# Kernel tuning notes

Hardware: AMD Instinct MI355X
Metric: run time of the kernel (lower is better)

Reference implementation:

```python
import jax, jax.numpy as jnp
import numpy as np

NUM_HEADS = 12
STEP_SIZE = 3

def softmax_1(a):
    # exp(a_i) / (1 + sum_j exp(a_j)), numerically stable
    m = jnp.maximum(jnp.max(a, axis=-1, keepdims=True), 0.0)
    e = jnp.exp(a - m)
    return e / (jnp.exp(-m) + jnp.sum(e, axis=-1, keepdims=True))

def setup_inputs() -> dict:
    key = jax.random.key(0)
    ks = jax.random.split(key, 7)
    B, N, C, L = 16, 4096, 768, 16
    s = C ** -0.5
    return {
        "x": jax.random.normal(ks[0], (B, N, C), dtype=jnp.float32),
        "query": jax.random.normal(ks[1], (1, L, C), dtype=jnp.float32),
        "Wq": jax.random.normal(ks[2], (C, C), dtype=jnp.float32) * s,
        "Wk": jax.random.normal(ks[3], (C, C), dtype=jnp.float32) * s,
        "Wv": jax.random.normal(ks[4], (C, C), dtype=jnp.float32) * s,
        "Wproj": jax.random.normal(ks[5], (C, C), dtype=jnp.float32) * s,
        "b_proj": jnp.zeros((C,), dtype=jnp.float32),
    }

def reference(x, query, Wq, Wk, Wv, Wproj, b_proj):
    B, N, C = x.shape
    H = NUM_HEADS
    hd = C // H
    L = query.shape[1]
    scale = hd ** -0.5
    # learned queries broadcast over batch
    queries = jnp.broadcast_to(query, (B, L, C))
    q = (queries @ Wq.T).reshape(B, L, H, hd).transpose(0, 2, 1, 3)  # [B,H,L,hd]
    k = (x @ Wk.T).reshape(B, N, H, hd).transpose(0, 2, 1, 3)        # [B,H,N,hd]
    v = k  # Hopfield update: state retrieves against stored patterns k
    for _ in range(STEP_SIZE):
        qs = q * scale
        attn = jnp.einsum('bhld,bhnd->bhln', qs, k)  # [B,H,L,N]
        attn = softmax_1(attn)
        q = jnp.einsum('bhln,bhnd->bhld', attn, v)   # [B,H,L,hd]
    out = q.transpose(0, 2, 1, 3).reshape(B, L, C)
    out = out @ Wv.T          # self.v output projection (no bias)
    out = out @ Wproj.T + b_proj  # self.proj
    return out
```

## Files before the change

### kernel.cpp

```cpp
#include <hip/hip_runtime.h>


typedef float  float4v  __attribute__((ext_vector_type(4)));
typedef short  short4v  __attribute__((ext_vector_type(4)));
typedef short  short8v  __attribute__((ext_vector_type(8)));
typedef unsigned int uint4v __attribute__((ext_vector_type(4)));
typedef short8v bf16x8;

#define NC 4

__device__ __forceinline__ unsigned short f2bf_hi(float f){
  unsigned int u = __float_as_uint(f);
  u += 0x7fffu + ((u >> 16) & 1u);
  return (unsigned short)(u >> 16);
}
__device__ __forceinline__ float bf2f(unsigned short h){
  return __uint_as_float(((unsigned int)h) << 16);
}
__device__ __forceinline__ unsigned int packbf(float v){
  unsigned short hh = f2bf_hi(v);
  return (unsigned)hh | ((unsigned)f2bf_hi(v - bf2f(hh)) << 16);
}

__global__ __launch_bounds__(256)
void cvt_planar_kernel(const float* __restrict__ src, unsigned short* __restrict__ dh,
                       unsigned short* __restrict__ dl){
  size_t idx = (size_t)blockIdx.x*256 + threadIdx.x;
  float4v v = ((const float4v*)src)[idx];
  short4v h4, l4;
  #pragma unroll
  for(int e=0;e<4;e++){
    unsigned short hh = f2bf_hi(v[e]);
    h4[e] = (short)hh;
    l4[e] = (short)f2bf_hi(v[e] - bf2f(hh));
  }
  ((short4v*)dh)[idx] = h4;
  ((short4v*)dl)[idx] = l4;
}

__global__ __launch_bounds__(256)
void q0_kernel(const float* __restrict__ query, const float* __restrict__ wq,
               float* __restrict__ q0){
  int idx = blockIdx.x*256 + threadIdx.x;
  int l = idx / 768, c = idx - l*768;
  const float* qr = query + l*768;
  const float* wr = wq + (size_t)c*768;
  float s = 0.f;
  for(int j=0;j<768;j+=4){
    float4v a  = *(const float4v*)(qr+j);
    float4v w4 = *(const float4v*)(wr+j);
    s += a[0]*w4[0]+a[1]*w4[1]+a[2]*w4[2]+a[3]*w4[3];
  }
  q0[idx] = s;
}

__global__ __launch_bounds__(256, 4)
void gemm_k_kernel(const float* __restrict__ x, const unsigned short* __restrict__ wh,
                   const unsigned short* __restrict__ wl, unsigned int* __restrict__ kout){
  __shared__ unsigned short Ah[128*40], Al[128*40];
  const int tid  = threadIdx.x;
  const int id   = blockIdx.x;
  const int xcd  = id & 7, slot = id >> 3;
  const int bml  = slot / 6;
  const int bn   = slot - bml*6;
  const int bm   = xcd*64 + bml;
  const int wave = tid >> 6, lane = tid & 63, quad = lane >> 4, l16 = lane & 15;

  float4v acc[8][2];
  #pragma unroll
  for(int i=0;i<8;i++)
    #pragma unroll
    for(int j=0;j<2;j++) acc[i][j] = (float4v){0.f,0.f,0.f,0.f};

  const float* xA = x + (size_t)bm*128*768;
  const unsigned short* wbh = wh + (size_t)(bn*128 + wave*32 + l16)*768 + quad*8;
  const unsigned short* wbl = wl + (size_t)(bn*128 + wave*32 + l16)*768 + quad*8;

  for(int k0=0;k0<768;k0+=32){
    bf16x8 b_h[2], b_l[2];
    #pragma unroll
    for(int j=0;j<2;j++){
      b_h[j] = *(const bf16x8*)(wbh + (size_t)j*16*768 + k0);
      b_l[j] = *(const bf16x8*)(wbl + (size_t)j*16*768 + k0);
    }
    __syncthreads();
    #pragma unroll
    for(int i=0;i<2;i++){
      int fi = tid + i*256;
      int row = fi >> 2, c8 = fi & 3;
      const float* sp = xA + (size_t)row*768 + k0 + c8*8;
      float4v va = *(const float4v*)sp;
      float4v vb = *(const float4v*)(sp + 4);
      short8v hv, lv;
      #pragma unroll
      for(int e=0;e<4;e++){
        unsigned short hh = f2bf_hi(va[e]);
        hv[e] = (short)hh; lv[e] = (short)f2bf_hi(va[e] - bf2f(hh));
        unsigned short hh2 = f2bf_hi(vb[e]);
        hv[e+4] = (short)hh2; lv[e+4] = (short)f2bf_hi(vb[e] - bf2f(hh2));
      }
      *(short8v*)(Ah + row*40 + c8*8) = hv;
      *(short8v*)(Al + row*40 + c8*8) = lv;
    }
    __syncthreads();

    #pragma unroll
    for(int i=0;i<8;i++){
      const int ar = i*16 + l16;
      bf16x8 a_h = *(const bf16x8*)(Ah + ar*40 + quad*8);
      bf16x8 a_l = *(const bf16x8*)(Al + ar*40 + quad*8);
      #pragma unroll
      for(int j=0;j<2;j++){
        acc[i][j] = __builtin_amdgcn_mfma_f32_16x16x32_bf16(a_h, b_h[j], acc[i][j],0,0,0);
        acc[i][j] = __builtin_amdgcn_mfma_f32_16x16x32_bf16(a_l, b_h[j], acc[i][j],0,0,0);
        acc[i][j] = __builtin_amdgcn_mfma_f32_16x16x32_bf16(a_h, b_l[j], acc[i][j],0,0,0);
      }
    }
  }
  const size_t cbase = (size_t)(bm*128)*768 + bn*128 + wave*32;
  #pragma unroll
  for(int i=0;i<8;i++)
    #pragma unroll
    for(int j=0;j<2;j++)
      #pragma unroll
      for(int r=0;r<4;r++)
        kout[cbase + (size_t)(i*16 + quad*4 + r)*768 + j*16 + l16] = packbf(acc[i][j][r]);
}

__global__ __launch_bounds__(256, 3)
void attn_step_kernel(const unsigned int* __restrict__ kbuf, const float* __restrict__ qsrc,
                      long qb_stride, float* __restrict__ qacc, float* __restrict__ lacc){
  __shared__ unsigned int knd[128*68];
  __shared__ float red[4][16];

  const int tid  = threadIdx.x;
  const int c    = blockIdx.x;
  const int h    = blockIdx.y;
  const int b    = blockIdx.z;
  const int wave = tid >> 6, lane = tid & 63, quad = lane >> 4, l16 = lane & 15;

  const unsigned int* kb = kbuf + ((size_t)b*4096 + (size_t)c*(4096/NC))*768 + h*64;

  const float* qp = qsrc + (size_t)b*qb_stride + (size_t)l16*768 + h*64;
  bf16x8 qh[2], ql[2];
  #pragma unroll
  for(int s = 0; s < 2; ++s){
    float4v v0 = *(const float4v*)(qp + s*32 + quad*8);
    float4v v1 = *(const float4v*)(qp + s*32 + quad*8 + 4);
    #pragma unroll
    for(int e = 0; e < 8; ++e){
      float v = (e < 4 ? v0[e] : v1[e-4]) * 0.125f;
      unsigned short hh = f2bf_hi(v);
      qh[s][e] = (short)hh;
      ql[s][e] = (short)f2bf_hi(v - bf2f(hh));
    }
  }

  float4v acc[4];
  #pragma unroll
  for(int j=0;j<4;j++) acc[j] = (float4v){0.f,0.f,0.f,0.f};
  float lsum = 0.f;

  const int prow = tid >> 1, pcol = (tid & 1)*32;
  const int T = (4096/NC)/128;
  uint4v pf[8];
  {
    const unsigned int* src = kb + (size_t)prow*768 + pcol;
    #pragma unroll
    for(int g=0; g<8; ++g) pf[g] = *(const uint4v*)(src + g*4);
  }

  const int rA = wave*32 + 8*(l16 >> 2) + (l16 & 3);

  for(int t = 0; t < T; ++t){
    #pragma unroll
    for(int g=0; g<8; ++g) *(uint4v*)(knd + prow*68 + pcol + g*4) = pf[g];
    __syncthreads();
    if(t+1 < T){
      const unsigned int* src = kb + (size_t)((t+1)*128 + prow)*768 + pcol;
      #pragma unroll
      for(int g=0; g<8; ++g) pf[g] = *(const uint4v*)(src + g*4);
    }

    float4v s1 = (float4v){0.f,0.f,0.f,0.f};
    float4v s2 = (float4v){0.f,0.f,0.f,0.f};
    #pragma unroll
    for(int s = 0; s < 2; ++s){
      const unsigned int* a1p = knd + rA*68 + s*32 + quad*8;
      const unsigned int* a2p = a1p + 4*68;
      uint4v w0 = *(const uint4v*)a1p;
      uint4v w1 = *(const uint4v*)(a1p + 4);
      uint4v u0 = *(const uint4v*)a2p;
      uint4v u1 = *(const uint4v*)(a2p + 4);
      bf16x8 a1h, a1l, a2h, a2l;
      #pragma unroll
      for(int j = 0; j < 4; ++j){
        a1h[j]   = (short)(w0[j] & 0xffffu);  a1l[j]   = (short)(w0[j] >> 16);
        a1h[j+4] = (short)(w1[j] & 0xffffu);  a1l[j+4] = (short)(w1[j] >> 16);
        a2h[j]   = (short)(u0[j] & 0xffffu);  a2l[j]   = (short)(u0[j] >> 16);
        a2h[j+4] = (short)(u1[j] & 0xffffu);  a2l[j+4] = (short)(u1[j] >> 16);
      }
      s1 = __builtin_amdgcn_mfma_f32_16x16x32_bf16(a1h, qh[s], s1, 0,0,0);
      s1 = __builtin_amdgcn_mfma_f32_16x16x32_bf16(a1l, qh[s], s1, 0,0,0);
      s1 = __builtin_amdgcn_mfma_f32_16x16x32_bf16(a1h, ql[s], s1, 0,0,0);
      s2 = __builtin_amdgcn_mfma_f32_16x16x32_bf16(a2h, qh[s], s2, 0,0,0);
      s2 = __builtin_amdgcn_mfma_f32_16x16x32_bf16(a2l, qh[s], s2, 0,0,0);
      s2 = __builtin_amdgcn_mfma_f32_16x16x32_bf16(a2h, ql[s], s2, 0,0,0);
    }

    bf16x8 pa_h, pa_l;
    #pragma unroll
    for(int e = 0; e < 4; ++e){
      float v = __expf(s1[e]);
      lsum += v;
      unsigned short hh = f2bf_hi(v);
      pa_h[e] = (short)hh;
      pa_l[e] = (short)f2bf_hi(v - bf2f(hh));
      float v2 = __expf(s2[e]);
      lsum += v2;
      unsigned short hh2 = f2bf_hi(v2);
      pa_h[e+4] = (short)hh2;
      pa_l[e+4] = (short)f2bf_hi(v2 - bf2f(hh2));
    }

    const unsigned int* bbase = knd + (size_t)(wave*32 + quad*8)*68 + l16;
    #pragma unroll
    for(int j = 0; j < 4; ++j){
      const unsigned int* bp = bbase + j*16;
      bf16x8 kbh, kbl;
      #pragma unroll
      for(int e = 0; e < 8; ++e){
        unsigned int w = bp[e*68];
        kbh[e] = (short)(w & 0xffffu);
        kbl[e] = (short)(w >> 16);
      }
      acc[j] = __builtin_amdgcn_mfma_f32_16x16x32_bf16(pa_h, kbh, acc[j], 0,0,0);
      acc[j] = __builtin_amdgcn_mfma_f32_16x16x32_bf16(pa_l, kbh, acc[j], 0,0,0);
      acc[j] = __builtin_amdgcn_mfma_f32_16x16x32_bf16(pa_h, kbl, acc[j], 0,0,0);
    }
    __syncthreads();
  }

  lsum += __shfl_xor(lsum, 16);
  lsum += __shfl_xor(lsum, 32);
  if(quad == 0) red[wave][l16] = lsum;
  __syncthreads();
  if(tid < 16){
    float tot = red[0][tid] + red[1][tid] + red[2][tid] + red[3][tid];
    atomicAdd(&lacc[(b*12 + h)*16 + tid], tot);
  }
  #pragma unroll
  for(int j = 0; j < 4; ++j)
    #pragma unroll
    for(int r = 0; r < 4; ++r)
      atomicAdd(&qacc[(size_t)(b*16 + quad*4 + r)*768 + h*64 + j*16 + l16], acc[j][r]);
}

__global__ __launch_bounds__(256)
void attn_norm_kernel(float* __restrict__ qacc, float* __restrict__ lacc,
                      float* __restrict__ qcur){
  __shared__ float lt[16];
  const int bh = blockIdx.x, b = bh/12, h = bh - (bh/12)*12, tid = threadIdx.x;
  if(tid < 16) lt[tid] = 1.f + lacc[bh*16 + tid];
  __syncthreads();
  if(tid < 16) lacc[bh*16 + tid] = 0.f;
  for(int idx = tid; idx < 1024; idx += 256){
    int l = idx >> 6, d = idx & 63;
    size_t a = (size_t)(b*16 + l)*768 + h*64 + d;
    qcur[a] = qacc[a] / lt[l];
    qacc[a] = 0.f;
  }
}

__global__ __launch_bounds__(256)
void proj_kernel(const float* __restrict__ inp, const float* __restrict__ w,
                 const float* __restrict__ bias, float* __restrict__ out){
  __shared__ float rows[4*768];
  const int r0 = blockIdx.x*4;
  const int c  = blockIdx.y*256 + threadIdx.x;
  for(int j = threadIdx.x; j < 4*768; j += 256) rows[j] = inp[(size_t)r0*768 + j];
  __syncthreads();
  const float* wr = w + (size_t)c*768;
  float a0=0.f, a1=0.f, a2=0.f, a3=0.f;
  for(int j=0;j<768;j+=4){
    float4v w4 = *(const float4v*)(wr+j);
    float4v r0v = *(const float4v*)(rows+j);
    float4v r1v = *(const float4v*)(rows+768+j);
    float4v r2v = *(const float4v*)(rows+1536+j);
    float4v r3v = *(const float4v*)(rows+2304+j);
    #pragma unroll
    for(int e=0;e<4;e++){
      a0 += r0v[e]*w4[e]; a1 += r1v[e]*w4[e];
      a2 += r2v[e]*w4[e]; a3 += r3v[e]*w4[e];
    }
  }
  const float bb = bias ? bias[c] : 0.f;
  out[(size_t)(r0+0)*768 + c] = a0 + bb;
  out[(size_t)(r0+1)*768 + c] = a1 + bb;
  out[(size_t)(r0+2)*768 + c] = a2 + bb;
  out[(size_t)(r0+3)*768 + c] = a3 + bb;
}

extern "C" void kernel_launch(void* const* d_in, const int* in_sizes, int n_in,
                              void* d_out, int out_size, void* d_ws, size_t ws_size,
                              hipStream_t stream){
  const float* x     = (const float*)d_in[0];
  const float* query = (const float*)d_in[1];
  const float* Wq    = (const float*)d_in[2];
  const float* Wk    = (const float*)d_in[3];
  const float* Wv    = (const float*)d_in[4];
  const float* Wproj = (const float*)d_in[5];
  const float* bproj = (const float*)d_in[6];
  float* out = (float*)d_out;

  char* ws = (char*)d_ws;
  unsigned int*   kbuf = (unsigned int*)(ws);
  float*          qcur = (float*)(ws + 201326592);
  float*          q0   = (float*)(ws + 202113024);
  char*           R    = ws + 202162176;
  unsigned short* wkh  = (unsigned short*)(R);
  unsigned short* wkl  = (unsigned short*)(R + 1179648);
  float*          qacc = (float*)(R);
  float*          lacc = (float*)(R + 786432);
  float*          out1 = (float*)(R);

  cvt_planar_kernel<<<576, 256, 0, stream>>>(Wk, wkh, wkl);
  q0_kernel<<<48, 256, 0, stream>>>(query, Wq, q0);
  gemm_k_kernel<<<3072, 256, 0, stream>>>(x, wkh, wkl, kbuf);

  hipMemsetAsync(qacc, 0, 786432 + 12288, stream);
  dim3 sg(NC, 12, 16);
  attn_step_kernel<<<sg, 256, 0, stream>>>(kbuf, q0,   0,       qacc, lacc);
  attn_norm_kernel<<<192, 256, 0, stream>>>(qacc, lacc, qcur);
  attn_step_kernel<<<sg, 256, 0, stream>>>(kbuf, qcur, 16*768,  qacc, lacc);
  attn_norm_kernel<<<192, 256, 0, stream>>>(qacc, lacc, qcur);
  attn_step_kernel<<<sg, 256, 0, stream>>>(kbuf, qcur, 16*768,  qacc, lacc);
  attn_norm_kernel<<<192, 256, 0, stream>>>(qacc, lacc, qcur);

  proj_kernel<<<dim3(64, 3), 256, 0, stream>>>(qcur, Wv, nullptr, out1);
  proj_kernel<<<dim3(64, 3), 256, 0, stream>>>(out1, Wproj, bproj, out);
}
```

Baseline: 749.2 us.

## Store K head-major and pre-split x to bf16 planes for LDS-free GEMM

The K projection output is now written in a per-(batch, head) contiguous layout, so each attention step reads fully contiguous 128x64 tiles instead of strided rows. The K GEMM drops the shared-memory staging of x and loads A and B fragments directly from global memory, using a 2x2 wave tiling with a larger per-wave register tile. When the workspace is large enough, x is first converted once into hi/lo bf16 planes so the GEMM does no per-tile conversion; otherwise a variant converts x inline. The trade is an extra full pass over x, about 200MB of extra workspace traffic, and higher register pressure.

```diff
diff --git a/kernel.cpp b/kernel.cpp
--- a/kernel.cpp
+++ b/kernel.cpp
@@ -54,10 +54,10 @@
   q0[idx] = s;
 }
 
-__global__ __launch_bounds__(256, 4)
-void gemm_k_kernel(const float* __restrict__ x, const unsigned short* __restrict__ wh,
-                   const unsigned short* __restrict__ wl, unsigned int* __restrict__ kout){
-  __shared__ unsigned short Ah[128*40], Al[128*40];
+__global__ __launch_bounds__(256, 3)
+void gemm_k_pre_kernel(const unsigned short* __restrict__ xh, const unsigned short* __restrict__ xl,
+                       const unsigned short* __restrict__ wh, const unsigned short* __restrict__ wl,
+                       unsigned int* __restrict__ khead){
   const int tid  = threadIdx.x;
   const int id   = blockIdx.x;
   const int xcd  = id & 7, slot = id >> 3;
@@ -65,70 +65,121 @@
   const int bn   = slot - bml*6;
   const int bm   = xcd*64 + bml;
   const int wave = tid >> 6, lane = tid & 63, quad = lane >> 4, l16 = lane & 15;
-
-  float4v acc[8][2];
-  #pragma unroll
-  for(int i=0;i<8;i++)
-    #pragma unroll
-    for(int j=0;j<2;j++) acc[i][j] = (float4v){0.f,0.f,0.f,0.f};
-
-  const float* xA = x + (size_t)bm*128*768;
-  const unsigned short* wbh = wh + (size_t)(bn*128 + wave*32 + l16)*768 + quad*8;
-  const unsigned short* wbl = wl + (size_t)(bn*128 + wave*32 + l16)*768 + quad*8;
+  const int wr   = wave >> 1, wc = wave & 1;
+
+  float4v acc[4][4];
+  #pragma unroll
+  for(int i=0;i<4;i++)
+    #pragma unroll
+    for(int j=0;j<4;j++) acc[i][j] = (float4v){0.f,0.f,0.f,0.f};
+
+  const size_t aoff = (size_t)(bm*128 + wr*64 + l16)*768 + quad*8;
+  const size_t boff = (size_t)(bn*128 + wc*64 + l16)*768 + quad*8;
+  const unsigned short* pah = xh + aoff;
+  const unsigned short* pal = xl + aoff;
+  const unsigned short* pbh = wh + boff;
+  const unsigned short* pbl = wl + boff;
 
   for(int k0=0;k0<768;k0+=32){
-    bf16x8 b_h[2], b_l[2];
-    #pragma unroll
-    for(int j=0;j<2;j++){
-      b_h[j] = *(const bf16x8*)(wbh + (size_t)j*16*768 + k0);
-      b_l[j] = *(const bf16x8*)(wbl + (size_t)j*16*768 + k0);
-    }
-    __syncthreads();
-    #pragma unroll
-    for(int i=0;i<2;i++){
-      int fi = tid + i*256;
-      int row = fi >> 2, c8 = fi & 3;
-      const float* sp = xA + (size_t)row*768 + k0 + c8*8;
+    bf16x8 ah[4], al[4], bh[4], bl[4];
+    #pragma unroll
+    for(int i=0;i<4;i++){
+      ah[i] = *(const bf16x8*)(pah + (size_t)i*16*768 + k0);
+      al[i] = *(const bf16x8*)(pal + (size_t)i*16*768 + k0);
+      bh[i] = *(const bf16x8*)(pbh + (size_t)i*16*768 + k0);
+      bl[i] = *(const bf16x8*)(pbl + (size_t)i*16*768 + k0);
+    }
+    #pragma unroll
+    for(int i=0;i<4;i++)
+      #pragma unroll
+      for(int j=0;j<4;j++){
+        acc[i][j] = __builtin_amdgcn_mfma_f32_16x16x32_bf16(ah[i], bh[j], acc[i][j],0,0,0);
+        acc[i][j] = __builtin_amdgcn_mfma_f32_16x16x32_bf16(al[i], bh[j], acc[i][j],0,0,0);
+        acc[i][j] = __builtin_amdgcn_mfma_f32_16x16x32_bf16(ah[i], bl[j], acc[i][j],0,0,0);
+      }
+  }
+  const int b     = bm >> 5;
+  const int h     = bn*2 + wc;
+  const int nbase = (bm & 31)*128 + wr*64;
+  unsigned int* kout = khead + (size_t)(b*12 + h)*4096*64;
+  #pragma unroll
+  for(int i=0;i<4;i++)
+    #pragma unroll
+    for(int j=0;j<4;j++)
+      #pragma unroll
+      for(int r=0;r<4;r++){
+        const int n = nbase + i*16 + quad*4 + r;
+        kout[(size_t)n*64 + j*16 + l16] = packbf(acc[i][j][r]);
+      }
+}
+
+__global__ __launch_bounds__(256, 3)
+void gemm_k_fly_kernel(const float* __restrict__ x,
+                       const unsigned short* __restrict__ wh, const unsigned short* __restrict__ wl,
+                       unsigned int* __restrict__ khead){
+  const int tid  = threadIdx.x;
+  const int id   = blockIdx.x;
+  const int xcd  = id & 7, slot = id >> 3;
+  const int bml  = slot / 6;
+  const int bn   = slot - bml*6;
+  const int bm   = xcd*64 + bml;
+  const int wave = tid >> 6, lane = tid & 63, quad = lane >> 4, l16 = lane & 15;
+  const int wr   = wave >> 1, wc = wave & 1;
+
+  float4v acc[4][4];
+  #pragma unroll
+  for(int i=0;i<4;i++)
+    #pragma unroll
+    for(int j=0;j<4;j++) acc[i][j] = (float4v){0.f,0.f,0.f,0.f};
+
+  const float* pax = x + (size_t)(bm*128 + wr*64 + l16)*768 + quad*8;
+  const size_t boff = (size_t)(bn*128 + wc*64 + l16)*768 + quad*8;
+  const unsigned short* pbh = wh + boff;
+  const unsigned short* pbl = wl + boff;
+
+  for(int k0=0;k0<768;k0+=32){
+    bf16x8 ah[4], al[4], bh[4], bl[4];
+    #pragma unroll
+    for(int i=0;i<4;i++){
+      const float* sp = pax + (size_t)i*16*768 + k0;
       float4v va = *(const float4v*)sp;
       float4v vb = *(const float4v*)(sp + 4);
-      short8v hv, lv;
       #pragma unroll
       for(int e=0;e<4;e++){
         unsigned short hh = f2bf_hi(va[e]);
-        hv[e] = (short)hh; lv[e] = (short)f2bf_hi(va[e] - bf2f(hh));
+        ah[i][e] = (short)hh; al[i][e] = (short)f2bf_hi(va[e] - bf2f(hh));
         unsigned short hh2 = f2bf_hi(vb[e]);
-        hv[e+4] = (short)hh2; lv[e+4] = (short)f2bf_hi(vb[e] - bf2f(hh2));
-      }
-      *(short8v*)(Ah + row*40 + c8*8) = hv;
-      *(short8v*)(Al + row*40 + c8*8) = lv;
-    }
-    __syncthreads();
-
-    #pragma unroll
-    for(int i=0;i<8;i++){
-      const int ar = i*16 + l16;
-      bf16x8 a_h = *(const bf16x8*)(Ah + ar*40 + quad*8);
-      bf16x8 a_l = *(const bf16x8*)(Al + ar*40 + quad*8);
-      #pragma unroll
-      for(int j=0;j<2;j++){
-        acc[i][j] = __builtin_amdgcn_mfma_f32_16x16x32_bf16(a_h, b_h[j], acc[i][j],0,0,0);
-        acc[i][j] = __builtin_amdgcn_mfma_f32_16x16x32_bf16(a_l, b_h[j], acc[i][j],0,0,0);
-        acc[i][j] = __builtin_amdgcn_mfma_f32_16x16x32_bf16(a_h, b_l[j], acc[i][j],0,0,0);
-      }
-    }
-  }
-  const size_t cbase = (size_t)(bm*128)*768 + bn*128 + wave*32;
-  #pragma unroll
-  for(int i=0;i<8;i++)
-    #pragma unroll
-    for(int j=0;j<2;j++)
-      #pragma unroll
-      for(int r=0;r<4;r++)
-        kout[cbase + (size_t)(i*16 + quad*4 + r)*768 + j*16 + l16] = packbf(acc[i][j][r]);
+        ah[i][e+4] = (short)hh2; al[i][e+4] = (short)f2bf_hi(vb[e] - bf2f(hh2));
+      }
+      bh[i] = *(const bf16x8*)(pbh + (size_t)i*16*768 + k0);
+      bl[i] = *(const bf16x8*)(pbl + (size_t)i*16*768 + k0);
+    }
+    #pragma unroll
+    for(int i=0;i<4;i++)
+      #pragma unroll
+      for(int j=0;j<4;j++){
+        acc[i][j] = __builtin_amdgcn_mfma_f32_16x16x32_bf16(ah[i], bh[j], acc[i][j],0,0,0);
+        acc[i][j] = __builtin_amdgcn_mfma_f32_16x16x32_bf16(al[i], bh[j], acc[i][j],0,0,0);
+        acc[i][j] = __builtin_amdgcn_mfma_f32_16x16x32_bf16(ah[i], bl[j], acc[i][j],0,0,0);
+      }
+  }
+  const int b     = bm >> 5;
+  const int h     = bn*2 + wc;
+  const int nbase = (bm & 31)*128 + wr*64;
+  unsigned int* kout = khead + (size_t)(b*12 + h)*4096*64;
+  #pragma unroll
+  for(int i=0;i<4;i++)
+    #pragma unroll
+    for(int j=0;j<4;j++)
+      #pragma unroll
+      for(int r=0;r<4;r++){
+        const int n = nbase + i*16 + quad*4 + r;
+        kout[(size_t)n*64 + j*16 + l16] = packbf(acc[i][j][r]);
+      }
 }
 
 __global__ __launch_bounds__(256, 3)
-void attn_step_kernel(const unsigned int* __restrict__ kbuf, const float* __restrict__ qsrc,
+void attn_step_kernel(const unsigned int* __restrict__ khead, const float* __restrict__ qsrc,
                       long qb_stride, float* __restrict__ qacc, float* __restrict__ lacc){
   __shared__ unsigned int knd[128*68];
   __shared__ float red[4][16];
@@ -139,7 +190,7 @@
   const int b    = blockIdx.z;
   const int wave = tid >> 6, lane = tid & 63, quad = lane >> 4, l16 = lane & 15;
 
-  const unsigned int* kb = kbuf + ((size_t)b*4096 + (size_t)c*(4096/NC))*768 + h*64;
+  const unsigned int* kb = khead + ((size_t)(b*12 + h)*4096 + (size_t)c*1024)*64;
 
   const float* qp = qsrc + (size_t)b*qb_stride + (size_t)l16*768 + h*64;
   bf16x8 qh[2], ql[2];
@@ -161,25 +212,26 @@
   for(int j=0;j<4;j++) acc[j] = (float4v){0.f,0.f,0.f,0.f};
   float lsum = 0.f;
 
-  const int prow = tid >> 1, pcol = (tid & 1)*32;
-  const int T = (4096/NC)/128;
+  const int srow = tid >> 4, scol = (tid & 15)*4;
+  const int T = (1024)/128;
   uint4v pf[8];
   {
-    const unsigned int* src = kb + (size_t)prow*768 + pcol;
-    #pragma unroll
-    for(int g=0; g<8; ++g) pf[g] = *(const uint4v*)(src + g*4);
+    const unsigned int* src = kb + tid*4;
+    #pragma unroll
+    for(int g=0; g<8; ++g) pf[g] = *(const uint4v*)(src + g*1024);
   }
 
   const int rA = wave*32 + 8*(l16 >> 2) + (l16 & 3);
 
   for(int t = 0; t < T; ++t){
     #pragma unroll
-    for(int g=0; g<8; ++g) *(uint4v*)(knd + prow*68 + pcol + g*4) = pf[g];
+    for(int g=0; g<8; ++g)
+      *(uint4v*)(knd + (g*16 + srow)*68 + scol) = pf[g];
     __syncthreads();
     if(t+1 < T){
-      const unsigned int* src = kb + (size_t)((t+1)*128 + prow)*768 + pcol;
-      #pragma unroll
-      for(int g=0; g<8; ++g) pf[g] = *(const uint4v*)(src + g*4);
+      const unsigned int* src = kb + (size_t)(t+1)*8192 + tid*4;
+      #pragma unroll
+      for(int g=0; g<8; ++g) pf[g] = *(const uint4v*)(src + g*1024);
     }
 
     float4v s1 = (float4v){0.f,0.f,0.f,0.f};
@@ -313,30 +365,65 @@
   const float* bproj = (const float*)d_in[6];
   float* out = (float*)d_out;
 
+  const size_t XB   = 100663296;
+  const size_t KB_  = 201326592;
+  const size_t PRE_NEED = 2*XB + KB_ + 786432 + 49152 + 2359296;
+
   char* ws = (char*)d_ws;
-  unsigned int*   kbuf = (unsigned int*)(ws);
-  float*          qcur = (float*)(ws + 201326592);
-  float*          q0   = (float*)(ws + 202113024);
-  char*           R    = ws + 202162176;
-  unsigned short* wkh  = (unsigned short*)(R);
-  unsigned short* wkl  = (unsigned short*)(R + 1179648);
-  float*          qacc = (float*)(R);
-  float*          lacc = (float*)(R + 786432);
-  float*          out1 = (float*)(R);
-
-  cvt_planar_kernel<<<576, 256, 0, stream>>>(Wk, wkh, wkl);
-  q0_kernel<<<48, 256, 0, stream>>>(query, Wq, q0);
-  gemm_k_kernel<<<3072, 256, 0, stream>>>(x, wkh, wkl, kbuf);
-
-  hipMemsetAsync(qacc, 0, 786432 + 12288, stream);
   dim3 sg(NC, 12, 16);
-  attn_step_kernel<<<sg, 256, 0, stream>>>(kbuf, q0,   0,       qacc, lacc);
-  attn_norm_kernel<<<192, 256, 0, stream>>>(qacc, lacc, qcur);
-  attn_step_kernel<<<sg, 256, 0, stream>>>(kbuf, qcur, 16*768,  qacc, lacc);
-  attn_norm_kernel<<<192, 256, 0, stream>>>(qacc, lacc, qcur);
-  attn_step_kernel<<<sg, 256, 0, stream>>>(kbuf, qcur, 16*768,  qacc, lacc);
-  attn_norm_kernel<<<192, 256, 0, stream>>>(qacc, lacc, qcur);
-
-  proj_kernel<<<dim3(64, 3), 256, 0, stream>>>(qcur, Wv, nullptr, out1);
-  proj_kernel<<<dim3(64, 3), 256, 0, stream>>>(out1, Wproj, bproj, out);
-}
+
+  if(ws_size >= PRE_NEED){
+    unsigned short* xh    = (unsigned short*)(ws);
+    unsigned short* xl    = (unsigned short*)(ws + XB);
+    unsigned int*   khead = (unsigned int*)  (ws + 2*XB);
+    float*          qcur  = (float*)(ws + 2*XB + KB_);
+    float*          q0    = (float*)(ws + 2*XB + KB_ + 786432);
+    char*           R     = ws + 2*XB + KB_ + 786432 + 49152;
+    unsigned short* wkh   = (unsigned short*)(R);
+    unsigned short* wkl   = (unsigned short*)(R + 1179648);
+    float*          qacc  = (float*)(R);
+    float*          lacc  = (float*)(R + 786432);
+    float*          out1  = (float*)(R);
+
+    cvt_planar_kernel<<<576, 256, 0, stream>>>(Wk, wkh, wkl);
+    cvt_planar_kernel<<<49152, 256, 0, stream>>>(x, xh, xl);
+    q0_kernel<<<48, 256, 0, stream>>>(query, Wq, q0);
+    gemm_k_pre_kernel<<<3072, 256, 0, stream>>>(xh, xl, wkh, wkl, khead);
+
+    hipMemsetAsync(qacc, 0, 786432 + 12288, stream);
+    attn_step_kernel<<<sg, 256, 0, stream>>>(khead, q0,   0,       qacc, lacc);
+    attn_norm_kernel<<<192, 256, 0, stream>>>(qacc, lacc, qcur);
+    attn_step_kernel<<<sg, 256, 0, stream>>>(khead, qcur, 16*768,  qacc, lacc);
+    attn_norm_kernel<<<192, 256, 0, stream>>>(qacc, lacc, qcur);
+    attn_step_kernel<<<sg, 256, 0, stream>>>(khead, qcur, 16*768,  qacc, lacc);
+    attn_norm_kernel<<<192, 256, 0, stream>>>(qacc, lacc, qcur);
+
+    proj_kernel<<<dim3(64, 3), 256, 0, stream>>>(qcur, Wv, nullptr, out1);
+    proj_kernel<<<dim3(64, 3), 256, 0, stream>>>(out1, Wproj, bproj, out);
+  } else {
+    unsigned int*   khead = (unsigned int*)(ws);
+    float*          qcur  = (float*)(ws + 201326592);
+    float*          q0    = (float*)(ws + 202113024);
+    char*           R     = ws + 202162176;
+    unsigned short* wkh   = (unsigned short*)(R);
+    unsigned short* wkl   = (unsigned short*)(R + 1179648);
+    float*          qacc  = (float*)(R);
+    float*          lacc  = (float*)(R + 786432);
+    float*          out1  = (float*)(R);
+
+    cvt_planar_kernel<<<576, 256, 0, stream>>>(Wk, wkh, wkl);
+    q0_kernel<<<48, 256, 0, stream>>>(query, Wq, q0);
+    gemm_k_fly_kernel<<<3072, 256, 0, stream>>>(x, wkh, wkl, khead);
+
+    hipMemsetAsync(qacc, 0, 786432 + 12288, stream);
+    attn_step_kernel<<<sg, 256, 0, stream>>>(khead, q0,   0,       qacc, lacc);
+    attn_norm_kernel<<<192, 256, 0, stream>>>(qacc, lacc, qcur);
+    attn_step_kernel<<<sg, 256, 0, stream>>>(khead, qcur, 16*768,  qacc, lacc);
+    attn_norm_kernel<<<192, 256, 0, stream>>>(qacc, lacc, qcur);
+    attn_step_kernel<<<sg, 256, 0, stream>>>(khead, qcur, 16*768,  qacc, lacc);
+    attn_norm_kernel<<<192, 256, 0, stream>>>(qacc, lacc, qcur);
+
+    proj_kernel<<<dim3(64, 3), 256, 0, stream>>>(qcur, Wv, nullptr, out1);
+    proj_kernel<<<dim3(64, 3), 256, 0, stream>>>(out1, Wproj, bproj, out);
+  }
+}
```

Result: slower. 1.083 ms (+44.5%).

## Fuse three Hopfield attention steps into one per-head kernel with head-major K

Applied to the files above, without the earlier changes.

The K projection output is now written in head-major layout [B,H,N,64], so each (batch, head) reads one contiguous slab. The three attention steps, their normalisations and the memset are merged into a single kernel with one 512-thread block per (b,h). That block loops over all N, reduces partial sums in shared memory, and keeps the updated query on-chip between iterations. This removes the atomics, the extra launches and the global round-trips of qacc and lacc, and adds an XOR-swizzled shared-memory layout to avoid bank conflicts. The cost is much less parallelism: only 192 blocks, each streaming the whole 4096-row K three times.

```diff
diff --git a/kernel.cpp b/kernel.cpp
--- a/kernel.cpp
+++ b/kernel.cpp
@@ -6,8 +6,6 @@
 typedef short  short8v  __attribute__((ext_vector_type(8)));
 typedef unsigned int uint4v __attribute__((ext_vector_type(4)));
 typedef short8v bf16x8;
-
-#define NC 4
 
 __device__ __forceinline__ unsigned short f2bf_hi(float f){
   unsigned int u = __float_as_uint(f);
@@ -56,7 +54,7 @@
 
 __global__ __launch_bounds__(256, 4)
 void gemm_k_kernel(const float* __restrict__ x, const unsigned short* __restrict__ wh,
-                   const unsigned short* __restrict__ wl, unsigned int* __restrict__ kout){
+                   const unsigned short* __restrict__ wl, unsigned int* __restrict__ khead){
   __shared__ unsigned short Ah[128*40], Al[128*40];
   const int tid  = threadIdx.x;
   const int id   = blockIdx.x;
@@ -117,158 +115,164 @@
       }
     }
   }
-  const size_t cbase = (size_t)(bm*128)*768 + bn*128 + wave*32;
+  const int b     = bm >> 5;
+  const int Cbase = bn*128 + wave*32;
+  const int h     = Cbase >> 6;
+  const int dbase = Cbase & 63;
+  const int nn0   = (bm & 31)*128;
+  unsigned int* kout = khead + ((size_t)(b*12 + h)*4096 + nn0)*64 + dbase;
   #pragma unroll
   for(int i=0;i<8;i++)
     #pragma unroll
     for(int j=0;j<2;j++)
       #pragma unroll
       for(int r=0;r<4;r++)
-        kout[cbase + (size_t)(i*16 + quad*4 + r)*768 + j*16 + l16] = packbf(acc[i][j][r]);
-}
-
-__global__ __launch_bounds__(256, 3)
-void attn_step_kernel(const unsigned int* __restrict__ kbuf, const float* __restrict__ qsrc,
-                      long qb_stride, float* __restrict__ qacc, float* __restrict__ lacc){
-  __shared__ unsigned int knd[128*68];
-  __shared__ float red[4][16];
+        kout[(size_t)(i*16 + quad*4 + r)*64 + j*16 + l16] = packbf(acc[i][j][r]);
+}
+
+__global__ __launch_bounds__(512, 2)
+void attn3_kernel(const unsigned int* __restrict__ khead,
+                  const float* __restrict__ q0g, float* __restrict__ qcur){
+  __shared__ unsigned int knd[256*64];
+  float* accf  = (float*)knd;
+  float* lredf = (float*)knd + 8192;
+  float* qtmp  = (float*)knd + 8320;
 
   const int tid  = threadIdx.x;
-  const int c    = blockIdx.x;
-  const int h    = blockIdx.y;
-  const int b    = blockIdx.z;
+  const int bh   = blockIdx.x;
+  const int b    = bh / 12;
+  const int h    = bh - b*12;
   const int wave = tid >> 6, lane = tid & 63, quad = lane >> 4, l16 = lane & 15;
 
-  const unsigned int* kb = kbuf + ((size_t)b*4096 + (size_t)c*(4096/NC))*768 + h*64;
-
-  const float* qp = qsrc + (size_t)b*qb_stride + (size_t)l16*768 + h*64;
-  bf16x8 qh[2], ql[2];
+  const unsigned int* kb = khead + (size_t)(b*12 + h)*4096*64;
+  const int srow = tid >> 1, scol = (tid & 1)*32;
+  const int sphi = ((srow & 7) << 2) ^ ((srow & 8) << 1);
+  const unsigned int* kbt = kb + (size_t)srow*64 + scol;
+
+  const int rowA = wave*32 + ((l16 >> 2) << 3) + (l16 & 3);
+  const int rowB = rowA + 4;
+  const int phiA = ((l16 & 3) << 2) ^ (((l16 >> 2) & 1) << 4);
+  const int phiB = phiA ^ 16;
+  const int q1   = quad & 1;
+
+  uint4v pf[8];
   #pragma unroll
-  for(int s = 0; s < 2; ++s){
-    float4v v0 = *(const float4v*)(qp + s*32 + quad*8);
-    float4v v1 = *(const float4v*)(qp + s*32 + quad*8 + 4);
-    #pragma unroll
-    for(int e = 0; e < 8; ++e){
-      float v = (e < 4 ? v0[e] : v1[e-4]) * 0.125f;
-      unsigned short hh = f2bf_hi(v);
-      qh[s][e] = (short)hh;
-      ql[s][e] = (short)f2bf_hi(v - bf2f(hh));
-    }
-  }
-
-  float4v acc[4];
-  #pragma unroll
-  for(int j=0;j<4;j++) acc[j] = (float4v){0.f,0.f,0.f,0.f};
-  float lsum = 0.f;
-
-  const int prow = tid >> 1, pcol = (tid & 1)*32;
-  const int T = (4096/NC)/128;
-  uint4v pf[8];
-  {
-    const unsigned int* src = kb + (size_t)prow*768 + pcol;
-    #pragma unroll
-    for(int g=0; g<8; ++g) pf[g] = *(const uint4v*)(src + g*4);
-  }
-
-  const int rA = wave*32 + 8*(l16 >> 2) + (l16 & 3);
-
-  for(int t = 0; t < T; ++t){
-    #pragma unroll
-    for(int g=0; g<8; ++g) *(uint4v*)(knd + prow*68 + pcol + g*4) = pf[g];
-    __syncthreads();
-    if(t+1 < T){
-      const unsigned int* src = kb + (size_t)((t+1)*128 + prow)*768 + pcol;
-      #pragma unroll
-      for(int g=0; g<8; ++g) pf[g] = *(const uint4v*)(src + g*4);
-    }
-
-    float4v s1 = (float4v){0.f,0.f,0.f,0.f};
-    float4v s2 = (float4v){0.f,0.f,0.f,0.f};
+  for(int g=0; g<8; ++g) pf[g] = *(const uint4v*)(kbt + g*4);
+
+  for(int iter = 0; iter < 3; ++iter){
+    const float* qrow = (iter == 0) ? (q0g + (size_t)l16*768 + h*64)
+                                    : (qtmp + l16*64);
+    bf16x8 qh[2], ql[2];
     #pragma unroll
     for(int s = 0; s < 2; ++s){
-      const unsigned int* a1p = knd + rA*68 + s*32 + quad*8;
-      const unsigned int* a2p = a1p + 4*68;
-      uint4v w0 = *(const uint4v*)a1p;
-      uint4v w1 = *(const uint4v*)(a1p + 4);
-      uint4v u0 = *(const uint4v*)a2p;
-      uint4v u1 = *(const uint4v*)(a2p + 4);
-      bf16x8 a1h, a1l, a2h, a2l;
+      float4v v0 = *(const float4v*)(qrow + s*32 + quad*8);
+      float4v v1 = *(const float4v*)(qrow + s*32 + quad*8 + 4);
+      #pragma unroll
+      for(int e = 0; e < 8; ++e){
+        float v = (e < 4 ? v0[e] : v1[e-4]) * 0.125f;
+        unsigned short hh = f2bf_hi(v);
+        qh[s][e] = (short)hh;
+        ql[s][e] = (short)f2bf_hi(v - bf2f(hh));
+      }
+    }
+    __syncthreads();
+
+    float4v acc[4];
+    #pragma unroll
+    for(int j=0;j<4;j++) acc[j] = (float4v){0.f,0.f,0.f,0.f};
+    float lsum = 0.f;
+
+    for(int t = 0; t < 16; ++t){
+      #pragma unroll
+      for(int g=0; g<8; ++g)
+        *(uint4v*)(knd + srow*64 + ((scol + g*4) ^ sphi)) = pf[g];
+      if(!(iter == 2 && t == 15)){
+        const int tn = (t + 1) & 15;
+        #pragma unroll
+        for(int g=0; g<8; ++g) pf[g] = *(const uint4v*)(kbt + (size_t)tn*16384 + g*4);
+      }
+
+      float4v s1 = (float4v){0.f,0.f,0.f,0.f};
+      float4v s2 = (float4v){0.f,0.f,0.f,0.f};
+      #pragma unroll
+      for(int s = 0; s < 2; ++s){
+        const int c0 = s*32 + quad*8;
+        uint4v w0 = *(const uint4v*)(knd + rowA*64 + ((c0    ) ^ phiA));
+        uint4v w1 = *(const uint4v*)(knd + rowA*64 + ((c0 + 4) ^ phiA));
+        uint4v u0 = *(const uint4v*)(knd + rowB*64 + ((c0    ) ^ phiB));
+        uint4v u1 = *(const uint4v*)(knd + rowB*64 + ((c0 + 4) ^ phiB));
+        bf16x8 a1h, a1l, a2h, a2l;
+        #pragma unroll
+        for(int j = 0; j < 4; ++j){
+          a1h[j]   = (short)(w0[j] & 0xffffu);  a1l[j]   = (short)(w0[j] >> 16);
+          a1h[j+4] = (short)(w1[j] & 0xffffu);  a1l[j+4] = (short)(w1[j] >> 16);
+          a2h[j]   = (short)(u0[j] & 0xffffu);  a2l[j]   = (short)(u0[j] >> 16);
+          a2h[j+4] = (short)(u1[j] & 0xffffu);  a2l[j+4] = (short)(u1[j] >> 16);
+        }
+        s1 = __builtin_amdgcn_mfma_f32_16x16x32_bf16(a1h, qh[s], s1, 0,0,0);
+        s1 = __builtin_amdgcn_mfma_f32_16x16x32_bf16(a1l, qh[s], s1, 0,0,0);
+        s1 = __builtin_amdgcn_mfma_f32_16x16x32_bf16(a1h, ql[s], s1, 0,0,0);
+        s2 = __builtin_amdgcn_mfma_f32_16x16x32_bf16(a2h, qh[s], s2, 0,0,0);
+        s2 = __builtin_amdgcn_mfma_f32_16x16x32_bf16(a2l, qh[s], s2, 0,0,0);
+        s2 = __builtin_amdgcn_mfma_f32_16x16x32_bf16(a2h, ql[s], s2, 0,0,0);
+      }
+
+      bf16x8 pa_h, pa_l;
+      #pragma unroll
+      for(int e = 0; e < 4; ++e){
+        float v = __expf(s1[e]);
+        lsum += v;
+        unsigned short hh = f2bf_hi(v);
+        pa_h[e] = (short)hh;
+        pa_l[e] = (short)f2bf_hi(v - bf2f(hh));
+        float v2 = __expf(s2[e]);
+        lsum += v2;
+        unsigned short hh2 = f2bf_hi(v2);
+        pa_h[e+4] = (short)hh2;
+        pa_l[e+4] = (short)f2bf_hi(v2 - bf2f(hh2));
+      }
+
+      const int rb0 = wave*32 + quad*8;
       #pragma unroll
       for(int j = 0; j < 4; ++j){
-        a1h[j]   = (short)(w0[j] & 0xffffu);  a1l[j]   = (short)(w0[j] >> 16);
-        a1h[j+4] = (short)(w1[j] & 0xffffu);  a1l[j+4] = (short)(w1[j] >> 16);
-        a2h[j]   = (short)(u0[j] & 0xffffu);  a2l[j]   = (short)(u0[j] >> 16);
-        a2h[j+4] = (short)(u1[j] & 0xffffu);  a2l[j+4] = (short)(u1[j] >> 16);
-      }
-      s1 = __builtin_amdgcn_mfma_f32_16x16x32_bf16(a1h, qh[s], s1, 0,0,0);
-      s1 = __builtin_amdgcn_mfma_f32_16x16x32_bf16(a1l, qh[s], s1, 0,0,0);
-      s1 = __builtin_amdgcn_mfma_f32_16x16x32_bf16(a1h, ql[s], s1, 0,0,0);
-      s2 = __builtin_amdgcn_mfma_f32_16x16x32_bf16(a2h, qh[s], s2, 0,0,0);
-      s2 = __builtin_amdgcn_mfma_f32_16x16x32_bf16(a2l, qh[s], s2, 0,0,0);
-      s2 = __builtin_amdgcn_mfma_f32_16x16x32_bf16(a2h, ql[s], s2, 0,0,0);
-    }
-
-    bf16x8 pa_h, pa_l;
-    #pragma unroll
-    for(int e = 0; e < 4; ++e){
-      float v = __expf(s1[e]);
-      lsum += v;
-      unsigned short hh = f2bf_hi(v);
-      pa_h[e] = (short)hh;
-      pa_l[e] = (short)f2bf_hi(v - bf2f(hh));
-      float v2 = __expf(s2[e]);
-      lsum += v2;
-      unsigned short hh2 = f2bf_hi(v2);
-      pa_h[e+4] = (short)hh2;
-      pa_l[e+4] = (short)f2bf_hi(v2 - bf2f(hh2));
-    }
-
-    const unsigned int* bbase = knd + (size_t)(wave*32 + quad*8)*68 + l16;
-    #pragma unroll
-    for(int j = 0; j < 4; ++j){
-      const unsigned int* bp = bbase + j*16;
-      bf16x8 kbh, kbl;
-      #pragma unroll
-      for(int e = 0; e < 8; ++e){
-        unsigned int w = bp[e*68];
-        kbh[e] = (short)(w & 0xffffu);
-        kbl[e] = (short)(w >> 16);
-      }
-      acc[j] = __builtin_amdgcn_mfma_f32_16x16x32_bf16(pa_h, kbh, acc[j], 0,0,0);
-      acc[j] = __builtin_amdgcn_mfma_f32_16x16x32_bf16(pa_l, kbh, acc[j], 0,0,0);
-      acc[j] = __builtin_amdgcn_mfma_f32_16x16x32_bf16(pa_h, kbl, acc[j], 0,0,0);
-    }
-    __syncthreads();
-  }
-
-  lsum += __shfl_xor(lsum, 16);
-  lsum += __shfl_xor(lsum, 32);
-  if(quad == 0) red[wave][l16] = lsum;
-  __syncthreads();
-  if(tid < 16){
-    float tot = red[0][tid] + red[1][tid] + red[2][tid] + red[3][tid];
-    atomicAdd(&lacc[(b*12 + h)*16 + tid], tot);
-  }
-  #pragma unroll
-  for(int j = 0; j < 4; ++j)
-    #pragma unroll
-    for(int r = 0; r < 4; ++r)
-      atomicAdd(&qacc[(size_t)(b*16 + quad*4 + r)*768 + h*64 + j*16 + l16], acc[j][r]);
-}
-
-__global__ __launch_bounds__(256)
-void attn_norm_kernel(float* __restrict__ qacc, float* __restrict__ lacc,
-                      float* __restrict__ qcur){
-  __shared__ float lt[16];
-  const int bh = blockIdx.x, b = bh/12, h = bh - (bh/12)*12, tid = threadIdx.x;
-  if(tid < 16) lt[tid] = 1.f + lacc[bh*16 + tid];
-  __syncthreads();
-  if(tid < 16) lacc[bh*16 + tid] = 0.f;
-  for(int idx = tid; idx < 1024; idx += 256){
-    int l = idx >> 6, d = idx & 63;
-    size_t a = (size_t)(b*16 + l)*768 + h*64 + d;
-    qcur[a] = qacc[a] / lt[l];
-    qacc[a] = 0.f;
+        bf16x8 kbh, kbl;
+        #pragma unroll
+        for(int e = 0; e < 8; ++e){
+          const int jx = ((e >> 2) ^ q1) & 1;
+          unsigned int w = knd[(rb0 + e)*64 + ((j ^ jx) << 4) + (l16 ^ ((e & 3) << 2))];
+          kbh[e] = (short)(w & 0xffffu);
+          kbl[e] = (short)(w >> 16);
+        }
+        acc[j] = __builtin_amdgcn_mfma_f32_16x16x32_bf16(pa_h, kbh, acc[j], 0,0,0);
+        acc[j] = __builtin_amdgcn_mfma_f32_16x16x32_bf16(pa_l, kbh, acc[j], 0,0,0);
+        acc[j] = __builtin_amdgcn_mfma_f32_16x16x32_bf16(pa_h, kbl, acc[j], 0,0,0);
+      }
+    }
+
+    __syncthreads();
+    lsum += __shfl_xor(lsum, 16);
+    lsum += __shfl_xor(lsum, 32);
+    if(quad == 0) lredf[wave*16 + l16] = lsum;
+    #pragma unroll
+    for(int j = 0; j < 4; ++j)
+      #pragma unroll
+      for(int r = 0; r < 4; ++r)
+        accf[wave*1024 + (quad*4 + r)*64 + j*16 + l16] = acc[j][r];
+    __syncthreads();
+    #pragma unroll
+    for(int k = 0; k < 2; ++k){
+      const int i = tid + k*512;
+      const int l = i >> 6, d = i & 63;
+      float s = 0.f, lt = 1.f;
+      #pragma unroll
+      for(int w = 0; w < 8; ++w){ s += accf[w*1024 + i]; }
+      #pragma unroll
+      for(int w = 0; w < 8; ++w){ lt += lredf[w*16 + l]; }
+      const float qv = s / lt;
+      if(iter < 2) qtmp[i] = qv;
+      else qcur[(size_t)(b*16 + l)*768 + h*64 + d] = qv;
+    }
+    __syncthreads();
   }
 }
 
@@ -314,28 +318,19 @@
   float* out = (float*)d_out;
 
   char* ws = (char*)d_ws;
-  unsigned int*   kbuf = (unsigned int*)(ws);
-  float*          qcur = (float*)(ws + 201326592);
-  float*          q0   = (float*)(ws + 202113024);
-  char*           R    = ws + 202162176;
-  unsigned short* wkh  = (unsigned short*)(R);
-  unsigned short* wkl  = (unsigned short*)(R + 1179648);
-  float*          qacc = (float*)(R);
-  float*          lacc = (float*)(R + 786432);
-  float*          out1 = (float*)(R);
+  unsigned int*   khead = (unsigned int*)(ws);
+  float*          qcur  = (float*)(ws + 201326592);
+  float*          q0    = (float*)(ws + 202113024);
+  char*           R     = ws + 202162176;
+  unsigned short* wkh   = (unsigned short*)(R);
+  unsigned short* wkl   = (unsigned short*)(R + 1179648);
+  float*          out1  = (float*)(R);
 
   cvt_planar_kernel<<<576, 256, 0, stream>>>(Wk, wkh, wkl);
   q0_kernel<<<48, 256, 0, stream>>>(query, Wq, q0);
-  gemm_k_kernel<<<3072, 256, 0, stream>>>(x, wkh, wkl, kbuf);
-
-  hipMemsetAsync(qacc, 0, 786432 + 12288, stream);
-  dim3 sg(NC, 12, 16);
-  attn_step_kernel<<<sg, 256, 0, stream>>>(kbuf, q0,   0,       qacc, lacc);
-  attn_norm_kernel<<<192, 256, 0, stream>>>(qacc, lacc, qcur);
-  attn_step_kernel<<<sg, 256, 0, stream>>>(kbuf, qcur, 16*768,  qacc, lacc);
-  attn_norm_kernel<<<192, 256, 0, stream>>>(qacc, lacc, qcur);
-  attn_step_kernel<<<sg, 256, 0, stream>>>(kbuf, qcur, 16*768,  qacc, lacc);
-  attn_norm_kernel<<<192, 256, 0, stream>>>(qacc, lacc, qcur);
+  gemm_k_kernel<<<3072, 256, 0, stream>>>(x, wkh, wkl, khead);
+
+  attn3_kernel<<<192, 512, 0, stream>>>(khead, q0, qcur);
 
   proj_kernel<<<dim3(64, 3), 256, 0, stream>>>(qcur, Wv, nullptr, out1);
   proj_kernel<<<dim3(64, 3), 256, 0, stream>>>(out1, Wproj, bproj, out);
```

Measured after the change: 709.9 us. 1.06x faster.
